# Kernel tuning notes

Measured on AMD Instinct MI355X. Metric: run time of the kernel, lower is better.

The kernel has to match this reference:

```python
import jax, jax.numpy as jnp
import numpy as np

B, N, P, H, E, M, O, T = 4, 128, 512, 64, 32, 64, 64, 64

def _normalize(v, axis=-1, eps=1e-12):
    n = jnp.sqrt(jnp.sum(v * v, axis=axis, keepdims=True))
    return v / jnp.maximum(n, eps)

def _quat_mul(a, b):
    aw, ax, ay, az = a[..., 0], a[..., 1], a[..., 2], a[..., 3]
    bw, bx, by, bz = b[..., 0], b[..., 1], b[..., 2], b[..., 3]
    return jnp.stack([
        aw*bw - ax*bx - ay*by - az*bz,
        aw*bx + ax*bw + ay*bz - az*by,
        aw*by - ax*bz + ay*bw + az*bx,
        aw*bz + ax*by - ay*bx + az*bw], axis=-1)

def _quat_conj(q):
    return q * jnp.array([1.0, -1.0, -1.0, -1.0], dtype=q.dtype)

def _quat_rotate(q, v):
    # rotate vectors v [...,3] by unit quaternions q [...,4] in (w,x,y,z)
    qv = q[..., 1:]
    w = q[..., :1]
    t = 2.0 * jnp.cross(qv, v)
    return v + w * t + jnp.cross(qv, t)

def _mlp(x, W1, b1, W2, b2):
    return jax.nn.relu(x @ W1 + b1) @ W2 + b2

def setup_inputs():
    key = jax.random.key(0)
    ks = jax.random.split(key, 20)
    def w(k, i, o):
        return (jax.random.normal(k, (i, o), jnp.float32) / np.sqrt(i)).astype(jnp.float32)
    inp = dict(
        q=_normalize(jax.random.normal(ks[0], (B, N, 4), jnp.float32)),
        x=jax.random.normal(ks[1], (B, N, 3), jnp.float32),
        torsions=jax.random.normal(ks[2], (B, N, 7, 2), jnp.float32),
        h=jax.random.normal(ks[3], (B, N, H), jnp.float32),
        e=jax.random.normal(ks[4], (B, N, N, E), jnp.float32),
        node_mask=jnp.ones((B, N), bool),
        pocket_q=_normalize(jax.random.normal(ks[5], (B, P, 4), jnp.float32)),
        pocket_x=jax.random.normal(ks[6], (B, P, 3), jnp.float32),
        pocket_e=jax.random.normal(ks[7], (B, N, P, E), jnp.float32),
        pocket_h=jax.random.normal(ks[8], (B, P, H), jnp.float32),
        pocket_mask=jnp.ones((B, P), bool),
        Wm1=w(ks[9], 2 * H + E + 9, T), bm1=jnp.zeros((T,), jnp.float32),
        Wm2=w(ks[10], T, M), bm2=jnp.zeros((M,), jnp.float32),
        Wf1=w(ks[11], H + M, T), bf1=jnp.zeros((T,), jnp.float32),
        Wf2=w(ks[12], T, O), bf2=jnp.zeros((O,), jnp.float32),
        Wx1=w(ks[13], M, T), bx1=jnp.zeros((T,), jnp.float32),
        Wx2=w(ks[14], T, 3), bx2=jnp.zeros((3,), jnp.float32),
        Wq1=w(ks[15], M, T), bq1=jnp.zeros((T,), jnp.float32),
        Wq2=w(ks[16], T, 4), bq2=jnp.zeros((4,), jnp.float32),
        Wt1=w(ks[17], M, T), bt1=jnp.zeros((T,), jnp.float32),
        Wt2=w(ks[18], T, 14), bt2=jnp.zeros((14,), jnp.float32),
    )
    return inp

def _forward(q, x, torsions, h, e, pocket_q, pocket_x, pocket_e, pocket_h,
             node_mask, pocket_mask,
             Wm1, bm1, Wm2, bm2, Wf1, bf1, Wf2, bf2,
             Wx1, bx1, Wx2, bx2, Wq1, bq1, Wq2, bq2, Wt1, bt1, Wt2, bt2):
    b, n, hd = h.shape
    p = pocket_h.shape[-2]
    eye = jnp.eye(n, dtype=bool)
    pep_mm = node_mask[:, :, None] & node_mask[:, None, :] & (~eye)[None]
    poc_mm = node_mask[:, :, None] & pocket_mask[:, None, :]
    msg_mask = jnp.concatenate([pep_mm, poc_mm], axis=-1).astype(h.dtype)  # [B,N,N+P]
    n_neigh = (node_mask.sum(-1) + pocket_mask.sum(-1) - 1).astype(h.dtype)

    all_x = jnp.concatenate([x, pocket_x], axis=-2)   # [B,N+P,3]
    all_q = jnp.concatenate([q, pocket_q], axis=-2)   # [B,N+P,4]

    diff = x[:, :, None, :] - all_x[:, None, :, :]    # [B,N,N+P,3]
    d2 = jnp.sum(diff * diff, axis=-1)                # [B,N,N+P] == cat(peptide_d2, pocket_d2)
    qdot = jnp.abs(jnp.sum(q[:, :, None, :] * all_q[:, None, :, :], axis=-1))
    conj_j = _quat_conj(all_q)[:, None, :, :]         # inverse of frame j rotation
    local_x = _quat_rotate(conj_j, diff)              # R_j^T (x_i - x_j): global_to_local.apply
    local_q = _quat_mul(conj_j, q[:, :, None, :])     # q_j^{-1} * q_i

    hi = jnp.broadcast_to(h[:, :, None, :], (b, n, n + p, hd))
    hj = jnp.broadcast_to(jnp.concatenate([h, pocket_h], axis=-2)[:, None, :, :], (b, n, n + p, hd))
    e_all = jnp.concatenate([e, pocket_e], axis=-2)

    feat = jnp.concatenate([hi, hj, e_all, local_x, local_q, d2[..., None], qdot[..., None]], axis=-1)
    m = _mlp(feat, Wm1, bm1, Wm2, bm2) * msg_mask[..., None]
    msum = m.sum(axis=-2)                             # [B,N,M]

    o = _mlp(jnp.concatenate([h, msum], axis=-1), Wf1, bf1, Wf2, bf2)
    upd_torsions = _normalize(_mlp(msum, Wt1, bt1, Wt2, bt2).reshape(torsions.shape))

    dx = _mlp(m, Wx1, bx1, Wx2, bx2) * msg_mask[..., None]
    dq = _mlp(msum, Wq1, bq1, Wq2, bq2)
    ident = jnp.array([1.0, 0.0, 0.0, 0.0], dtype=dq.dtype)
    dq = jnp.where(node_mask[..., None], dq, ident)
    dq = _normalize(dq)
    upd_q = _quat_mul(q, dq)
    upd_q = jnp.where(node_mask[..., None], upd_q, ident)
    upd_q = _normalize(upd_q)                         # Rigid(Rotation(..., normalize_quats=True))

    rot_j = _normalize(all_q)[:, None, :, :]          # local->global rotation, normalize_quats=True
    upd_x = x + _quat_rotate(rot_j, dx).sum(axis=-2) / n_neigh[:, None, None]
    return upd_q, upd_x, upd_torsions, o

def reference(q, x, torsions, h, e, node_mask, pocket_q, pocket_x, pocket_e, pocket_h, pocket_mask,
              Wm1, bm1, Wm2, bm2, Wf1, bf1, Wf2, bf2,
              Wx1, bx1, Wx2, bx2, Wq1, bq1, Wq2, bq2, Wt1, bt1, Wt2, bt2):
    return _forward(q, x, torsions, h, e, pocket_q, pocket_x, pocket_e, pocket_h,
                    node_mask, pocket_mask,
                    Wm1, bm1, Wm2, bm2, Wf1, bf1, Wf2, bf2,
                    Wx1, bx1, Wx2, bx2, Wq1, bq1, Wq2, bq2, Wt1, bt1, Wt2, bt2)
```

## Files before the change

kernel.cpp:

```cpp
#include <hip/hip_runtime.h>
#include <stdint.h>

#define NB 4
#define NN 128
#define NP 512
#define HD 64
#define ED 32

typedef unsigned short u16;
typedef __attribute__((ext_vector_type(8))) short short8;
typedef __attribute__((ext_vector_type(4))) float f32x4;

#define OFF_Q 0
#define OFF_X 2048
#define OFF_T 3584
#define OFF_O 10752

__device__ __forceinline__ uint32_t cvtpk(float a, float b) {
  uint32_t r;
  asm("v_cvt_pk_bf16_f32 %0, %1, %2" : "=v"(r) : "v"(a), "v"(b));
  return r;
}
__device__ __forceinline__ u16 bfh(float a) { return (u16)cvtpk(a, 0.f); }

__device__ __forceinline__ int w1row(int k) {
  if (k < 32) return 128 + k;
  if (k < 35) return 160 + (k - 32);
  if (k < 39) return 163 + (k - 35);
  if (k == 39) return 167;
  if (k == 40) return 168;
  if (k < 48) return -1;
  if (k < 112) return 64 + (k - 48);
  return -1;
}

struct TileRegs {
  float4 e0, e1, h0, h1, h2, h3, qj;
  float xj0, xj1, xj2;
};

__global__ void __launch_bounds__(256, 2)
egnn_fused(const float* __restrict__ q, const float* __restrict__ x,
           const float* __restrict__ h, const float* __restrict__ e,
           const float* __restrict__ pe, const float* __restrict__ pq,
           const float* __restrict__ px, const float* __restrict__ ph,
           const float* __restrict__ Wm1, const float* __restrict__ bm1,
           const float* __restrict__ Wm2, const float* __restrict__ bm2,
           const float* __restrict__ Wx1, const float* __restrict__ bx1,
           const float* __restrict__ Wx2, const float* __restrict__ bx2,
           const float* __restrict__ Wf1, const float* __restrict__ bf1,
           const float* __restrict__ Wf2, const float* __restrict__ bf2_,
           const float* __restrict__ Wq1, const float* __restrict__ bq1,
           const float* __restrict__ Wq2, const float* __restrict__ bq2,
           const float* __restrict__ Wt1, const float* __restrict__ bt1,
           const float* __restrict__ Wt2, const float* __restrict__ bt2,
           float* __restrict__ out)
{
  __shared__ __align__(16) u16 sW1B[64 * 128];
  __shared__ __align__(16) u16 sW2B[64 * 72];
  __shared__ __align__(16) u16 sWx1B[64 * 72];
  __shared__ __align__(16) u16 sWx2B[16 * 72];
  __shared__ __align__(16) u16 sF[4][16 * 128];
  __shared__ __align__(16) u16 sT[4][16 * 64];
  __shared__ float sDxT[4][16][4];
  __shared__ float sMsum[4][64];
  __shared__ float sDx[4][3];
  __shared__ float sHi64[64];
  __shared__ float sHiP[64];
  __shared__ float sPh3[4][64];

  const int b = blockIdx.x >> 7;
  const int i = blockIdx.x & 127;
  const int tid = threadIdx.x;
  const int wid = tid >> 6;
  const int lane = tid & 63;
  const int nl = lane & 15;
  const int quad = lane >> 4;
  const size_t node = (size_t)(b * NN + i);

  u16* sFw = sF[wid];
  u16* sTw = sT[wid];

  auto tload = [&](TileRegs& R, int jb) {
    int er = lane >> 2, c = lane & 3;
    int jr = jb + er;
    const float* ebase = (jr < NN)
        ? e + ((node * NN) + jr) * ED + c * 8
        : pe + ((node * NP) + (jr - NN)) * ED + c * 8;
    R.e0 = *(const float4*)ebase;
    R.e1 = *(const float4*)(ebase + 4);
    const float* hb = (jr < NN) ? h + ((size_t)(b * NN + jr)) * HD + c * 16
                                : ph + ((size_t)(b * NP + (jr - NN))) * HD + c * 16;
    R.h0 = *(const float4*)hb;
    R.h1 = *(const float4*)(hb + 4);
    R.h2 = *(const float4*)(hb + 8);
    R.h3 = *(const float4*)(hb + 12);
    if (lane < 16) {
      int j = jb + lane;
      const float* qr = (j < NN) ? q + ((size_t)(b * NN + j)) * 4
                                 : pq + ((size_t)(b * NP + (j - NN))) * 4;
      R.qj = *(const float4*)qr;
      const float* xr = (j < NN) ? x + ((size_t)(b * NN + j)) * 3
                                 : px + ((size_t)(b * NP + (j - NN))) * 3;
      R.xj0 = xr[0]; R.xj1 = xr[1]; R.xj2 = xr[2];
    }
  };

  TileRegs RA, RB;
  tload(RA, wid * 16);

  for (int idx = tid; idx < 64 * 128; idx += 256) {
    int n = idx >> 7, k = idx & 127;
    int row = w1row(k);
    sW1B[n * 128 + (k ^ ((n & 7) << 3))] =
        (row < 0) ? (u16)0 : bfh(Wm1[(size_t)row * 64 + n]);
  }
  for (int idx = tid; idx < 64 * 64; idx += 256) {
    int n = idx >> 6, k = idx & 63;
    sW2B[n * 72 + k]  = bfh(Wm2[(size_t)k * 64 + n]);
    sWx1B[n * 72 + k] = bfh(Wx1[(size_t)k * 64 + n]);
  }
  for (int idx = tid; idx < 16 * 64; idx += 256) {
    int n = idx >> 6, k = idx & 63;
    sWx2B[n * 72 + k] = (n < 3) ? bfh(Wx2[(size_t)k * 3 + n]) : (u16)0;
  }
  for (int idx = lane; idx < 16 * 128 / 2; idx += 64) ((uint32_t*)sFw)[idx] = 0;

  if (tid < 64) sHi64[tid] = h[node * HD + tid];
  if (tid >= 64 && tid < 128) {
    int col = tid - 64;
    float acc = bm1[col];
#pragma unroll 8
    for (int k = 0; k < HD; ++k) acc += h[node * HD + k] * Wm1[k * 64 + col];
    sHiP[col] = acc;
  }

  const float* qr0 = q + node * 4;
  const float qi0 = qr0[0], qi1 = qr0[1], qi2 = qr0[2], qi3 = qr0[3];
  const float* xr0 = x + node * 3;
  const float xi0 = xr0[0], xi1 = xr0[1], xi2 = xr0[2];

  __syncthreads();

  short8 W2f[4][2], Wx1f[4][2], Wx2f[2];
#pragma unroll
  for (int nt = 0; nt < 4; ++nt)
#pragma unroll
    for (int ks = 0; ks < 2; ++ks) {
      W2f[nt][ks]  = *(const short8*)&sW2B[(nt * 16 + nl) * 72 + ks * 32 + quad * 8];
      Wx1f[nt][ks] = *(const short8*)&sWx1B[(nt * 16 + nl) * 72 + ks * 32 + quad * 8];
    }
#pragma unroll
  for (int ks = 0; ks < 2; ++ks)
    Wx2f[ks] = *(const short8*)&sWx2B[nl * 72 + ks * 32 + quad * 8];

  float HiF[4], bm2F[4], bx1F[4];
#pragma unroll
  for (int nt = 0; nt < 4; ++nt) {
    HiF[nt] = sHiP[nt * 16 + nl];
    bm2F[nt] = bm2[nt * 16 + nl];
    bx1F[nt] = bx1[nt * 16 + nl];
  }
  const float bx2F = (nl < 3) ? bx2[nl] : 0.f;

  f32x4 msum[4];
#pragma unroll
  for (int nt = 0; nt < 4; ++nt) msum[nt] = (f32x4){0.f, 0.f, 0.f, 0.f};
  float dxs0 = 0.f, dxs1 = 0.f, dxs2 = 0.f;

  const int swr = (nl & 7) << 3;

  auto process = [&](const TileRegs& R, int jb) {
    const int er = lane >> 2, c = lane & 3;
    {
      const int sw = (er & 7) << 3;
      uint4 pw;
      pw.x = cvtpk(R.e0.x, R.e0.y); pw.y = cvtpk(R.e0.z, R.e0.w);
      pw.z = cvtpk(R.e1.x, R.e1.y); pw.w = cvtpk(R.e1.z, R.e1.w);
      *(uint4*)&sFw[er * 128 + ((c * 8) ^ sw)] = pw;
      uint4 pa, pb;
      pa.x = cvtpk(R.h0.x, R.h0.y); pa.y = cvtpk(R.h0.z, R.h0.w);
      pa.z = cvtpk(R.h1.x, R.h1.y); pa.w = cvtpk(R.h1.z, R.h1.w);
      pb.x = cvtpk(R.h2.x, R.h2.y); pb.y = cvtpk(R.h2.z, R.h2.w);
      pb.z = cvtpk(R.h3.x, R.h3.y); pb.w = cvtpk(R.h3.z, R.h3.w);
      *(uint4*)&sFw[er * 128 + ((48 + c * 16) ^ sw)] = pa;
      *(uint4*)&sFw[er * 128 + ((56 + c * 16) ^ sw)] = pb;
    }
    float nqw = 0.f, nqx = 0.f, nqy = 0.f, nqz = 0.f;
    if (lane < 16) {
      const float4 qj = R.qj;
      const float xj0 = R.xj0, xj1 = R.xj1, xj2 = R.xj2;
      float d0 = xi0 - xj0, d1 = xi1 - xj1, d2v = xi2 - xj2;
      float d2 = d0 * d0 + d1 * d1 + d2v * d2v;
      float qdot = fabsf(qi0 * qj.x + qi1 * qj.y + qi2 * qj.z + qi3 * qj.w);
      float ajw = qj.x, ajx = -qj.y, ajy = -qj.z, ajz = -qj.w;
      float t0 = 2.f * (ajy * d2v - ajz * d1);
      float t1 = 2.f * (ajz * d0 - ajx * d2v);
      float t2 = 2.f * (ajx * d1 - ajy * d0);
      float lx0 = d0 + ajw * t0 + (ajy * t2 - ajz * t1);
      float lx1 = d1 + ajw * t1 + (ajz * t0 - ajx * t2);
      float lx2 = d2v + ajw * t2 + (ajx * t1 - ajy * t0);
      float lqw = ajw * qi0 - ajx * qi1 - ajy * qi2 - ajz * qi3;
      float lqx = ajw * qi1 + ajx * qi0 + ajy * qi3 - ajz * qi2;
      float lqy = ajw * qi2 - ajx * qi3 + ajy * qi0 + ajz * qi1;
      float lqz = ajw * qi3 + ajx * qi2 - ajy * qi1 + ajz * qi0;
      float nn2 = qj.x * qj.x + qj.y * qj.y + qj.z * qj.z + qj.w * qj.w;
      float rn = 1.f / fmaxf(sqrtf(nn2), 1e-12f);
      nqw = qj.x * rn; nqx = qj.y * rn; nqy = qj.z * rn; nqz = qj.w * rn;
      uint4 g0, g1;
      g0.x = cvtpk(lx0, lx1); g0.y = cvtpk(lx2, lqw);
      g0.z = cvtpk(lqx, lqy); g0.w = cvtpk(lqz, d2);
      g1.x = cvtpk(qdot, 0.f); g1.y = 0; g1.z = 0; g1.w = 0;
      const int sw = (lane & 7) << 3;
      *(uint4*)&sFw[lane * 128 + (32 ^ sw)] = g0;
      *(uint4*)&sFw[lane * 128 + (40 ^ sw)] = g1;
    }

    f32x4 acc[4];
#pragma unroll
    for (int nt = 0; nt < 4; ++nt)
      acc[nt] = (f32x4){HiF[nt], HiF[nt], HiF[nt], HiF[nt]};
#pragma unroll
    for (int ks = 0; ks < 4; ++ks) {
      const int ko = (ks * 32 + quad * 8) ^ swr;
      short8 af = *(const short8*)&sFw[nl * 128 + ko];
#pragma unroll
      for (int nt = 0; nt < 4; ++nt) {
        short8 bfr = *(const short8*)&sW1B[(nt * 16 + nl) * 128 + ko];
        acc[nt] = __builtin_amdgcn_mfma_f32_16x16x32_bf16(af, bfr, acc[nt], 0, 0, 0);
      }
    }
#pragma unroll
    for (int r = 0; r < 4; ++r) {
      const int row = quad * 4 + r;
      const int sw2 = (row & 7) << 3;
#pragma unroll
      for (int nt = 0; nt < 4; ++nt)
        sTw[row * 64 + ((nt * 16 + nl) ^ sw2)] = bfh(fmaxf(acc[nt][r], 0.f));
    }

#pragma unroll
    for (int nt = 0; nt < 4; ++nt)
      acc[nt] = (f32x4){bm2F[nt], bm2F[nt], bm2F[nt], bm2F[nt]};
#pragma unroll
    for (int ks = 0; ks < 2; ++ks) {
      const int ko = (ks * 32 + quad * 8) ^ swr;
      short8 af = *(const short8*)&sTw[nl * 64 + ko];
#pragma unroll
      for (int nt = 0; nt < 4; ++nt)
        acc[nt] = __builtin_amdgcn_mfma_f32_16x16x32_bf16(af, W2f[nt][ks], acc[nt], 0, 0, 0);
    }
#pragma unroll
    for (int r = 0; r < 4; ++r) {
      const int row = quad * 4 + r;
      const int sw2 = (row & 7) << 3;
#pragma unroll
      for (int nt = 0; nt < 4; ++nt) {
        float v = acc[nt][r];
        if (jb + row == i) v = 0.f;
        msum[nt][r] += v;
        sTw[row * 64 + ((nt * 16 + nl) ^ sw2)] = bfh(v);
      }
    }

#pragma unroll
    for (int nt = 0; nt < 4; ++nt)
      acc[nt] = (f32x4){bx1F[nt], bx1F[nt], bx1F[nt], bx1F[nt]};
#pragma unroll
    for (int ks = 0; ks < 2; ++ks) {
      const int ko = (ks * 32 + quad * 8) ^ swr;
      short8 af = *(const short8*)&sTw[nl * 64 + ko];
#pragma unroll
      for (int nt = 0; nt < 4; ++nt)
        acc[nt] = __builtin_amdgcn_mfma_f32_16x16x32_bf16(af, Wx1f[nt][ks], acc[nt], 0, 0, 0);
    }
#pragma unroll
    for (int r = 0; r < 4; ++r) {
      const int row = quad * 4 + r;
      const int sw2 = (row & 7) << 3;
#pragma unroll
      for (int nt = 0; nt < 4; ++nt)
        sTw[row * 64 + ((nt * 16 + nl) ^ sw2)] = bfh(fmaxf(acc[nt][r], 0.f));
    }

    f32x4 dacc = (f32x4){bx2F, bx2F, bx2F, bx2F};
#pragma unroll
    for (int ks = 0; ks < 2; ++ks) {
      const int ko = (ks * 32 + quad * 8) ^ swr;
      short8 af = *(const short8*)&sTw[nl * 64 + ko];
      dacc = __builtin_amdgcn_mfma_f32_16x16x32_bf16(af, Wx2f[ks], dacc, 0, 0, 0);
    }
    if (nl < 3) {
#pragma unroll
      for (int r = 0; r < 4; ++r) sDxT[wid][quad * 4 + r][nl] = dacc[r];
    }
    if (lane < 16) {
      int j = jb + lane;
      if (j != i) {
        float dxc0 = sDxT[wid][lane][0];
        float dxc1 = sDxT[wid][lane][1];
        float dxc2 = sDxT[wid][lane][2];
        float rt0 = 2.f * (nqy * dxc2 - nqz * dxc1);
        float rt1 = 2.f * (nqz * dxc0 - nqx * dxc2);
        float rt2 = 2.f * (nqx * dxc1 - nqy * dxc0);
        dxs0 += dxc0 + nqw * rt0 + (nqy * rt2 - nqz * rt1);
        dxs1 += dxc1 + nqw * rt1 + (nqz * rt0 - nqx * rt2);
        dxs2 += dxc2 + nqw * rt2 + (nqx * rt1 - nqy * rt0);
      }
    }
  };

  for (int t = 0; t < 10; t += 2) {
    const int k0 = wid + t * 4;
    tload(RB, (k0 + 4) * 16);
    process(RA, k0 * 16);
    if (t + 2 < 10) tload(RA, (k0 + 8) * 16);
    process(RB, (k0 + 4) * 16);
  }

#pragma unroll
  for (int nt = 0; nt < 4; ++nt) {
    float s = msum[nt][0] + msum[nt][1] + msum[nt][2] + msum[nt][3];
    s += __shfl_xor(s, 16);
    s += __shfl_xor(s, 32);
    if (lane < 16) sMsum[wid][nt * 16 + lane] = s;
  }
  {
    float a = dxs0, bb = dxs1, cc = dxs2;
#pragma unroll
    for (int off = 1; off < 16; off <<= 1) {
      a += __shfl_xor(a, off);
      bb += __shfl_xor(bb, off);
      cc += __shfl_xor(cc, off);
    }
    if (lane == 0) { sDx[wid][0] = a; sDx[wid][1] = bb; sDx[wid][2] = cc; }
  }
  __syncthreads();

  if (wid == 0) {
    float ms = sMsum[0][lane] + sMsum[1][lane] + sMsum[2][lane] + sMsum[3][lane];
    sPh3[0][lane] = ms;
    float f1a = bf1[lane], f1b = 0.f;
#pragma unroll 8
    for (int k = 0; k < 64; ++k) {
      f1a += sHi64[k] * Wf1[k * 64 + lane];
      f1b += sPh3[0][k] * Wf1[(64 + k) * 64 + lane];
    }
    float f1 = fmaxf(f1a + f1b, 0.f);
    sPh3[0][lane] = f1;
    float oacc = bf2_[lane];
#pragma unroll 8
    for (int k = 0; k < 64; ++k) oacc += sPh3[0][k] * Wf2[k * 64 + lane];
    out[OFF_O + node * 64 + lane] = oacc;
  } else if (wid == 1) {
    float ms = sMsum[0][lane] + sMsum[1][lane] + sMsum[2][lane] + sMsum[3][lane];
    sPh3[1][lane] = ms;
    float a = bq1[lane];
#pragma unroll 8
    for (int k = 0; k < 64; ++k) a += sPh3[1][k] * Wq1[k * 64 + lane];
    a = fmaxf(a, 0.f);
    float p0 = a * Wq2[lane * 4 + 0];
    float p1 = a * Wq2[lane * 4 + 1];
    float p2 = a * Wq2[lane * 4 + 2];
    float p3 = a * Wq2[lane * 4 + 3];
#pragma unroll
    for (int off = 32; off >= 1; off >>= 1) {
      p0 += __shfl_xor(p0, off);
      p1 += __shfl_xor(p1, off);
      p2 += __shfl_xor(p2, off);
      p3 += __shfl_xor(p3, off);
    }
    float dq0 = p0 + bq2[0], dq1 = p1 + bq2[1];
    float dq2 = p2 + bq2[2], dq3 = p3 + bq2[3];
    float n = fmaxf(sqrtf(dq0 * dq0 + dq1 * dq1 + dq2 * dq2 + dq3 * dq3), 1e-12f);
    dq0 /= n; dq1 /= n; dq2 /= n; dq3 /= n;
    float uw = qi0 * dq0 - qi1 * dq1 - qi2 * dq2 - qi3 * dq3;
    float ux = qi0 * dq1 + qi1 * dq0 + qi2 * dq3 - qi3 * dq2;
    float uy = qi0 * dq2 - qi1 * dq3 + qi2 * dq0 + qi3 * dq1;
    float uz = qi0 * dq3 + qi1 * dq2 - qi2 * dq1 + qi3 * dq0;
    float n2 = fmaxf(sqrtf(uw * uw + ux * ux + uy * uy + uz * uz), 1e-12f);
    if (lane == 0) {
      float* po = out + OFF_Q + node * 4;
      po[0] = uw / n2; po[1] = ux / n2; po[2] = uy / n2; po[3] = uz / n2;
    }
  } else if (wid == 2) {
    float ms = sMsum[0][lane] + sMsum[1][lane] + sMsum[2][lane] + sMsum[3][lane];
    sPh3[2][lane] = ms;
    float a = bt1[lane];
#pragma unroll 8
    for (int k = 0; k < 64; ++k) a += sPh3[2][k] * Wt1[k * 64 + lane];
    a = fmaxf(a, 0.f);
    sPh3[2][lane] = a;
    if (lane < 14) {
      float v = bt2[lane];
#pragma unroll 8
      for (int k = 0; k < 64; ++k) v += sPh3[2][k] * Wt2[k * 14 + lane];
      float pv = __shfl_xor(v, 1);
      float nrm = fmaxf(sqrtf(v * v + pv * pv), 1e-12f);
      out[OFF_T + node * 14 + lane] = v / nrm;
    }
  } else {
    if (lane < 3) {
      float xs = sDx[0][lane] + sDx[1][lane] + sDx[2][lane] + sDx[3][lane];
      float xiv = (lane == 0) ? xi0 : (lane == 1) ? xi1 : xi2;
      out[OFF_X + node * 3 + lane] = xiv + xs / 639.0f;
    }
  }
}

extern "C" void kernel_launch(void* const* d_in, const int* in_sizes, int n_in,
                              void* d_out, int out_size, void* d_ws, size_t ws_size,
                              hipStream_t stream) {
  const float* q   = (const float*)d_in[0];
  const float* x   = (const float*)d_in[1];
  const float* h   = (const float*)d_in[3];
  const float* e   = (const float*)d_in[4];
  const float* pq  = (const float*)d_in[6];
  const float* px  = (const float*)d_in[7];
  const float* pe  = (const float*)d_in[8];
  const float* ph  = (const float*)d_in[9];
  const float* Wm1 = (const float*)d_in[11];
  const float* bm1 = (const float*)d_in[12];
  const float* Wm2 = (const float*)d_in[13];
  const float* bm2 = (const float*)d_in[14];
  const float* Wf1 = (const float*)d_in[15];
  const float* bf1 = (const float*)d_in[16];
  const float* Wf2 = (const float*)d_in[17];
  const float* bf2_ = (const float*)d_in[18];
  const float* Wx1 = (const float*)d_in[19];
  const float* bx1 = (const float*)d_in[20];
  const float* Wx2 = (const float*)d_in[21];
  const float* bx2 = (const float*)d_in[22];
  const float* Wq1 = (const float*)d_in[23];
  const float* bq1 = (const float*)d_in[24];
  const float* Wq2 = (const float*)d_in[25];
  const float* bq2 = (const float*)d_in[26];
  const float* Wt1 = (const float*)d_in[27];
  const float* bt1 = (const float*)d_in[28];
  const float* Wt2 = (const float*)d_in[29];
  const float* bt2 = (const float*)d_in[30];

  egnn_fused<<<NB * NN, 256, 0, stream>>>(
      q, x, h, e, pe, pq, px, ph,
      Wm1, bm1, Wm2, bm2, Wx1, bx1, Wx2, bx2,
      Wf1, bf1, Wf2, bf2_, Wq1, bq1, Wq2, bq2,
      Wt1, bt1, Wt2, bt2, (float*)d_out);
}
```

Baseline: 224.7 us.

## Cut registers and LDS to raise occupancy to three blocks per SIMD

Removes the shared-memory staging of the W2, Wx1 and Wx2 weights. Each lane now loads and packs its bf16 MFMA fragments straight from global memory. The double-buffered register tiles are replaced by a single-tile loop that prefetches only the edge features for the next tile, while h, q and x are loaded in the same iteration they are used. Launch bounds go from 2 to 3 blocks per multiprocessor to raise occupancy and hide latency. The cost is less software prefetch of the h/q/x loads and some redundant strided global weight reads per block.

```diff
diff --git a/kernel.cpp b/kernel.cpp
--- a/kernel.cpp
+++ b/kernel.cpp
@@ -22,6 +22,15 @@
   return r;
 }
 __device__ __forceinline__ u16 bfh(float a) { return (u16)cvtpk(a, 0.f); }
+
+__device__ __forceinline__ short8 pack8(const float v[8]) {
+  union { uint32_t u[4]; short8 s; } cv;
+  cv.u[0] = cvtpk(v[0], v[1]);
+  cv.u[1] = cvtpk(v[2], v[3]);
+  cv.u[2] = cvtpk(v[4], v[5]);
+  cv.u[3] = cvtpk(v[6], v[7]);
+  return cv.s;
+}
 
 __device__ __forceinline__ int w1row(int k) {
   if (k < 32) return 128 + k;
@@ -34,12 +43,7 @@
   return -1;
 }
 
-struct TileRegs {
-  float4 e0, e1, h0, h1, h2, h3, qj;
-  float xj0, xj1, xj2;
-};
-
-__global__ void __launch_bounds__(256, 2)
+__global__ void __launch_bounds__(256, 3)
 egnn_fused(const float* __restrict__ q, const float* __restrict__ x,
            const float* __restrict__ h, const float* __restrict__ e,
            const float* __restrict__ pe, const float* __restrict__ pq,
@@ -57,9 +61,6 @@
            float* __restrict__ out)
 {
   __shared__ __align__(16) u16 sW1B[64 * 128];
-  __shared__ __align__(16) u16 sW2B[64 * 72];
-  __shared__ __align__(16) u16 sWx1B[64 * 72];
-  __shared__ __align__(16) u16 sWx2B[16 * 72];
   __shared__ __align__(16) u16 sF[4][16 * 128];
   __shared__ __align__(16) u16 sT[4][16 * 64];
   __shared__ float sDxT[4][16][4];
@@ -81,33 +82,19 @@
   u16* sFw = sF[wid];
   u16* sTw = sT[wid];
 
-  auto tload = [&](TileRegs& R, int jb) {
-    int er = lane >> 2, c = lane & 3;
+  const int er = lane >> 2, ec = lane & 3;
+
+  auto eload = [&](float4& A, float4& Bv, int jb) {
     int jr = jb + er;
-    const float* ebase = (jr < NN)
-        ? e + ((node * NN) + jr) * ED + c * 8
-        : pe + ((node * NP) + (jr - NN)) * ED + c * 8;
-    R.e0 = *(const float4*)ebase;
-    R.e1 = *(const float4*)(ebase + 4);
-    const float* hb = (jr < NN) ? h + ((size_t)(b * NN + jr)) * HD + c * 16
-                                : ph + ((size_t)(b * NP + (jr - NN))) * HD + c * 16;
-    R.h0 = *(const float4*)hb;
-    R.h1 = *(const float4*)(hb + 4);
-    R.h2 = *(const float4*)(hb + 8);
-    R.h3 = *(const float4*)(hb + 12);
-    if (lane < 16) {
-      int j = jb + lane;
-      const float* qr = (j < NN) ? q + ((size_t)(b * NN + j)) * 4
-                                 : pq + ((size_t)(b * NP + (j - NN))) * 4;
-      R.qj = *(const float4*)qr;
-      const float* xr = (j < NN) ? x + ((size_t)(b * NN + j)) * 3
-                                 : px + ((size_t)(b * NP + (j - NN))) * 3;
-      R.xj0 = xr[0]; R.xj1 = xr[1]; R.xj2 = xr[2];
-    }
+    const float* eb = (jr < NN)
+        ? e + ((node * NN) + jr) * ED + ec * 8
+        : pe + ((node * NP) + (jr - NN)) * ED + ec * 8;
+    A = *(const float4*)eb;
+    Bv = *(const float4*)(eb + 4);
   };
 
-  TileRegs RA, RB;
-  tload(RA, wid * 16);
+  float4 EA, EB;
+  eload(EA, EB, wid * 16);
 
   for (int idx = tid; idx < 64 * 128; idx += 256) {
     int n = idx >> 7, k = idx & 127;
@@ -115,15 +102,6 @@
     sW1B[n * 128 + (k ^ ((n & 7) << 3))] =
         (row < 0) ? (u16)0 : bfh(Wm1[(size_t)row * 64 + n]);
   }
-  for (int idx = tid; idx < 64 * 64; idx += 256) {
-    int n = idx >> 6, k = idx & 63;
-    sW2B[n * 72 + k]  = bfh(Wm2[(size_t)k * 64 + n]);
-    sWx1B[n * 72 + k] = bfh(Wx1[(size_t)k * 64 + n]);
-  }
-  for (int idx = tid; idx < 16 * 64; idx += 256) {
-    int n = idx >> 6, k = idx & 63;
-    sWx2B[n * 72 + k] = (n < 3) ? bfh(Wx2[(size_t)k * 3 + n]) : (u16)0;
-  }
   for (int idx = lane; idx < 16 * 128 / 2; idx += 64) ((uint32_t*)sFw)[idx] = 0;
 
   if (tid < 64) sHi64[tid] = h[node * HD + tid];
@@ -140,29 +118,44 @@
   const float* xr0 = x + node * 3;
   const float xi0 = xr0[0], xi1 = xr0[1], xi2 = xr0[2];
 
-  __syncthreads();
-
   short8 W2f[4][2], Wx1f[4][2], Wx2f[2];
 #pragma unroll
   for (int nt = 0; nt < 4; ++nt)
 #pragma unroll
     for (int ks = 0; ks < 2; ++ks) {
-      W2f[nt][ks]  = *(const short8*)&sW2B[(nt * 16 + nl) * 72 + ks * 32 + quad * 8];
-      Wx1f[nt][ks] = *(const short8*)&sWx1B[(nt * 16 + nl) * 72 + ks * 32 + quad * 8];
-    }
-#pragma unroll
-  for (int ks = 0; ks < 2; ++ks)
-    Wx2f[ks] = *(const short8*)&sWx2B[nl * 72 + ks * 32 + quad * 8];
-
-  float HiF[4], bm2F[4], bx1F[4];
+      const int n = nt * 16 + nl, k0 = ks * 32 + quad * 8;
+      float v2[8], vx[8];
+#pragma unroll
+      for (int r = 0; r < 8; ++r) {
+        v2[r] = Wm2[(size_t)(k0 + r) * 64 + n];
+        vx[r] = Wx1[(size_t)(k0 + r) * 64 + n];
+      }
+      W2f[nt][ks] = pack8(v2);
+      Wx1f[nt][ks] = pack8(vx);
+    }
+#pragma unroll
+  for (int ks = 0; ks < 2; ++ks) {
+    const int k0 = ks * 32 + quad * 8;
+    float v[8];
+#pragma unroll
+    for (int r = 0; r < 8; ++r) v[r] = (nl < 3) ? Wx2[(size_t)(k0 + r) * 3 + nl] : 0.f;
+    Wx2f[ks] = pack8(v);
+  }
+
+  float bm2F[4], bx1F[4];
 #pragma unroll
   for (int nt = 0; nt < 4; ++nt) {
-    HiF[nt] = sHiP[nt * 16 + nl];
     bm2F[nt] = bm2[nt * 16 + nl];
     bx1F[nt] = bx1[nt * 16 + nl];
   }
   const float bx2F = (nl < 3) ? bx2[nl] : 0.f;
 
+  __syncthreads();
+
+  float HiF[4];
+#pragma unroll
+  for (int nt = 0; nt < 4; ++nt) HiF[nt] = sHiP[nt * 16 + nl];
+
   f32x4 msum[4];
 #pragma unroll
   for (int nt = 0; nt < 4; ++nt) msum[nt] = (f32x4){0.f, 0.f, 0.f, 0.f};
@@ -170,26 +163,50 @@
 
   const int swr = (nl & 7) << 3;
 
-  auto process = [&](const TileRegs& R, int jb) {
-    const int er = lane >> 2, c = lane & 3;
+  for (int t = 0; t < 10; ++t) {
+    const int jb = (wid + t * 4) * 16;
+
+    const int jr = jb + er;
+    const float* hb = (jr < NN) ? h + ((size_t)(b * NN + jr)) * HD + ec * 16
+                                : ph + ((size_t)(b * NP + (jr - NN))) * HD + ec * 16;
+    float4 h0 = *(const float4*)hb;
+    float4 h1 = *(const float4*)(hb + 4);
+    float4 h2 = *(const float4*)(hb + 8);
+    float4 h3 = *(const float4*)(hb + 12);
+    float4 qj;
+    float xj0 = 0.f, xj1 = 0.f, xj2 = 0.f;
+    if (lane < 16) {
+      int j = jb + lane;
+      const float* qr = (j < NN) ? q + ((size_t)(b * NN + j)) * 4
+                                 : pq + ((size_t)(b * NP + (j - NN))) * 4;
+      qj = *(const float4*)qr;
+      const float* xr = (j < NN) ? x + ((size_t)(b * NN + j)) * 3
+                                 : px + ((size_t)(b * NP + (j - NN))) * 3;
+      xj0 = xr[0]; xj1 = xr[1]; xj2 = xr[2];
+    }
+
     {
       const int sw = (er & 7) << 3;
       uint4 pw;
-      pw.x = cvtpk(R.e0.x, R.e0.y); pw.y = cvtpk(R.e0.z, R.e0.w);
-      pw.z = cvtpk(R.e1.x, R.e1.y); pw.w = cvtpk(R.e1.z, R.e1.w);
-      *(uint4*)&sFw[er * 128 + ((c * 8) ^ sw)] = pw;
+      pw.x = cvtpk(EA.x, EA.y); pw.y = cvtpk(EA.z, EA.w);
+      pw.z = cvtpk(EB.x, EB.y); pw.w = cvtpk(EB.z, EB.w);
+      *(uint4*)&sFw[er * 128 + ((ec * 8) ^ sw)] = pw;
+    }
+    if (t < 9) eload(EA, EB, (wid + (t + 1) * 4) * 16);
+
+    {
+      const int sw = (er & 7) << 3;
       uint4 pa, pb;
-      pa.x = cvtpk(R.h0.x, R.h0.y); pa.y = cvtpk(R.h0.z, R.h0.w);
-      pa.z = cvtpk(R.h1.x, R.h1.y); pa.w = cvtpk(R.h1.z, R.h1.w);
-      pb.x = cvtpk(R.h2.x, R.h2.y); pb.y = cvtpk(R.h2.z, R.h2.w);
-      pb.z = cvtpk(R.h3.x, R.h3.y); pb.w = cvtpk(R.h3.z, R.h3.w);
-      *(uint4*)&sFw[er * 128 + ((48 + c * 16) ^ sw)] = pa;
-      *(uint4*)&sFw[er * 128 + ((56 + c * 16) ^ sw)] = pb;
-    }
+      pa.x = cvtpk(h0.x, h0.y); pa.y = cvtpk(h0.z, h0.w);
+      pa.z = cvtpk(h1.x, h1.y); pa.w = cvtpk(h1.z, h1.w);
+      pb.x = cvtpk(h2.x, h2.y); pb.y = cvtpk(h2.z, h2.w);
+      pb.z = cvtpk(h3.x, h3.y); pb.w = cvtpk(h3.z, h3.w);
+      *(uint4*)&sFw[er * 128 + ((48 + ec * 16) ^ sw)] = pa;
+      *(uint4*)&sFw[er * 128 + ((56 + ec * 16) ^ sw)] = pb;
+    }
+
     float nqw = 0.f, nqx = 0.f, nqy = 0.f, nqz = 0.f;
     if (lane < 16) {
-      const float4 qj = R.qj;
-      const float xj0 = R.xj0, xj1 = R.xj1, xj2 = R.xj2;
       float d0 = xi0 - xj0, d1 = xi1 - xj1, d2v = xi2 - xj2;
       float d2 = d0 * d0 + d1 * d1 + d2v * d2v;
       float qdot = fabsf(qi0 * qj.x + qi1 * qj.y + qi2 * qj.z + qi3 * qj.w);
@@ -308,14 +325,6 @@
         dxs2 += dxc2 + nqw * rt2 + (nqx * rt1 - nqy * rt0);
       }
     }
-  };
-
-  for (int t = 0; t < 10; t += 2) {
-    const int k0 = wid + t * 4;
-    tload(RB, (k0 + 4) * 16);
-    process(RA, k0 * 16);
-    if (t + 2 < 10) tload(RA, (k0 + 8) * 16);
-    process(RB, (k0 + 4) * 16);
   }
 
 #pragma unroll
```

New measurement: 242.5 us. +7.9%, slower.
